# Performance work log

Measured on AMD Instinct MI355X. Metric: run time of the kernel, lower is better.

Reference implementation:

```python
import jax, jax.numpy as jnp
import numpy as np

NL = 4      # num_hidden_layers
NH = 12     # self-attn heads
CH = 4      # cross-attn heads (hardcoded in module)
S = 4       # speakers per dialog
EPS = 1e-5

def layernorm(x, g, b):
    m = x.mean(-1, keepdims=True)
    v = jnp.mean((x - m) ** 2, axis=-1, keepdims=True)
    return (x - m) * jax.lax.rsqrt(v + EPS) * g + b

def self_mha(x, in_w, in_b, out_w, out_b):
    # x: [B,T,L,H] self-attention over L (the per-turn token axis)
    B, T, L, H = x.shape
    dh = H // NH
    qkv = x @ in_w + in_b                       # [B,T,L,3H]
    q, k, v = jnp.split(qkv, 3, axis=-1)
    q = q.reshape(B, T, L, NH, dh); k = k.reshape(B, T, L, NH, dh); v = v.reshape(B, T, L, NH, dh)
    s = jnp.einsum('btqhd,btkhd->bthqk', q, k) / np.sqrt(dh).astype(x.dtype)
    a = jax.nn.softmax(s, axis=-1)
    o = jnp.einsum('bthqk,btkhd->btqhd', a, v).reshape(B, T, L, H)
    return o @ out_w + out_b

def forward(input_ids, attention_mask, speaker_ids, tok_emb, pos_emb, turn_emb,
            mha_in_w, mha_in_b, mha_out_w, mha_out_b,
            ffn_w1, ffn_b1, ffn_w2, ffn_b2,
            ln1_g, ln1_b, ln2_g, ln2_b,
            gate_w, gate_b, sn_g, sn_b,
            ca_in_w, ca_in_b, ca_out_w, ca_out_b):
    B, T, L = input_ids.shape
    H = tok_emb.shape[1]
    X = tok_emb[input_ids] + pos_emb[jnp.arange(L)][None, None] + turn_emb[jnp.arange(T)][None, :, None]
    mask = attention_mask[..., None].astype(X.dtype)            # [B,T,L,1]
    onehot = (speaker_ids[..., None] == jnp.arange(S)).astype(X.dtype)  # [B,T,S]
    counts = onehot.sum(1)                                      # [B,S]
    M = jnp.zeros((B, S, H), X.dtype)                           # speaker memory
    for l in range(NL):
        m_t = jnp.einsum('bts,bsh->bth', onehot, M)             # gather memory per turn
        h = (X + m_t[:, :, None, :]) * mask                     # mask applied by zeroing inputs (as in source)
        h = self_mha(h, mha_in_w[l], mha_in_b[l], mha_out_w[l], mha_out_b[l])
        h = layernorm(h + X, ln1_g[l], ln1_b[l])
        ffn = jax.nn.gelu(h @ ffn_w1[l] + ffn_b1[l], approximate=False) @ ffn_w2[l] + ffn_b2[l]
        h = layernorm(h + ffn, ln2_g[l], ln2_b[l])
        X = h
        tc = h.mean(2)                                          # token_context [B,T,H]
        # cross-attention: each turn's context queries its dialog's speaker memory
        wq, wk, wv = jnp.split(ca_in_w[l], 3, axis=-1)
        bq, bk, bv = jnp.split(ca_in_b[l], 3)
        dh = H // CH
        q = (tc @ wq + bq).reshape(B, T, CH, dh)
        k = (M @ wk + bk).reshape(B, S, CH, dh)
        v = (M @ wv + bv).reshape(B, S, CH, dh)
        s = jnp.einsum('bthd,bshd->bhts', q, k) / np.sqrt(dh).astype(X.dtype)
        a = jax.nn.softmax(s, axis=-1)
        cc = jnp.einsum('bhts,bshd->bthd', a, v).reshape(B, T, H) @ ca_out_w[l] + ca_out_b[l]
        fused = jnp.concatenate([tc, m_t, cc], axis=-1)         # [B,T,3H]
        upd = layernorm(fused @ gate_w[l] + gate_b[l] + m_t, sn_g[l], sn_b[l])
        # scatter: per-speaker mean over that speaker's turns; untouched speakers keep old memory
        sums = jnp.einsum('bts,bth->bsh', onehot, upd)
        mean = sums / jnp.maximum(counts, 1.0)[..., None]
        M = jnp.where((counts > 0)[..., None], mean, M)
    return X, M

def setup_inputs() -> dict:
    key = jax.random.key(0)
    ks = iter(jax.random.split(key, 32))
    B, T, L, H, F, V, P = 8, 64, 64, 768, 3072, 30522, 512
    n = lambda shape: jax.random.normal(next(ks), shape, jnp.float32) * 0.02
    return {
        'input_ids': jax.random.randint(next(ks), (B, T, L), 0, V, jnp.int32),
        'attention_mask': jax.random.randint(next(ks), (B, T, L), 0, 2, jnp.int32),
        'speaker_ids': jax.random.randint(next(ks), (B, T), 0, S, jnp.int32),
        'tok_emb': n((V, H)), 'pos_emb': n((P, H)), 'turn_emb': n((P, H)),
        'mha_in_w': n((NL, H, 3 * H)), 'mha_in_b': jnp.zeros((NL, 3 * H)),
        'mha_out_w': n((NL, H, H)), 'mha_out_b': jnp.zeros((NL, H)),
        'ffn_w1': n((NL, H, F)), 'ffn_b1': jnp.zeros((NL, F)),
        'ffn_w2': n((NL, F, H)), 'ffn_b2': jnp.zeros((NL, H)),
        'ln1_g': jnp.ones((NL, H)), 'ln1_b': jnp.zeros((NL, H)),
        'ln2_g': jnp.ones((NL, H)), 'ln2_b': jnp.zeros((NL, H)),
        'gate_w': n((NL, 3 * H, H)), 'gate_b': jnp.zeros((NL, H)),
        'sn_g': jnp.ones((NL, H)), 'sn_b': jnp.zeros((NL, H)),
        'ca_in_w': n((NL, H, 3 * H)), 'ca_in_b': jnp.zeros((NL, 3 * H)),
        'ca_out_w': n((NL, H, H)), 'ca_out_b': jnp.zeros((NL, H)),
    }

def reference(input_ids, attention_mask, speaker_ids, tok_emb, pos_emb, turn_emb,
              mha_in_w, mha_in_b, mha_out_w, mha_out_b,
              ffn_w1, ffn_b1, ffn_w2, ffn_b2,
              ln1_g, ln1_b, ln2_g, ln2_b,
              gate_w, gate_b, sn_g, sn_b,
              ca_in_w, ca_in_b, ca_out_w, ca_out_b):
    return forward(input_ids, attention_mask, speaker_ids, tok_emb, pos_emb, turn_emb,
                   mha_in_w, mha_in_b, mha_out_w, mha_out_b,
                   ffn_w1, ffn_b1, ffn_w2, ffn_b2,
                   ln1_g, ln1_b, ln2_g, ln2_b,
                   gate_w, gate_b, sn_g, sn_b,
                   ca_in_w, ca_in_b, ca_out_w, ca_out_b)
```

## Files before the change

kernel.cpp:

```cpp
#include <hip/hip_runtime.h>

using u16 = unsigned short;
using u32 = unsigned int;

#define DI __device__ __forceinline__

typedef __bf16 bf16x8 __attribute__((ext_vector_type(8)));
typedef float  f32x4  __attribute__((ext_vector_type(4)));

DI float b2f(u16 u){ u32 x = ((u32)u) << 16; float f; __builtin_memcpy(&f, &x, 4); return f; }
DI u16 f2b(float f){ __bf16 h = (__bf16)f; u16 r; __builtin_memcpy(&r, &h, 2); return r; }
DI float gelu_fast(float v){
    float u = v * (0.7978845608f + 0.0356774081f * v * v);
    float e = __expf(2.0f * u);
    float t = 1.0f - 2.0f / (e + 1.0f);
    return 0.5f * v * (1.0f + t);
}

#define GLOAD16(g, l) __builtin_amdgcn_global_load_lds( \
    (const __attribute__((address_space(1))) void*)(g), \
    (__attribute__((address_space(3))) void*)(l), 16, 0, 0)

DI bf16x8 ldsr128(const u16* p) {
    bf16x8 r;
    asm volatile("ds_read_b128 %0, %1"
                 : "=v"(r)
                 : "v"((const __attribute__((address_space(3))) u16*)p));
    return r;
}

template<int EPI>
__global__ __launch_bounds__(512, 1)
void gemm256(const u16* __restrict__ A, const u16* __restrict__ Bt,
             const float* __restrict__ bias, void* __restrict__ Cout,
             int M, int N, int K)
{
    __shared__ u16 lA[2][256 * 64];
    __shared__ u16 lB[2][256 * 64];
    const int tid  = threadIdx.x;
    const int lane = tid & 63;
    const int w    = tid >> 6;
    const int wm   = w >> 2, wn = w & 3;

    const int nx = gridDim.x;
    const int nb = nx * gridDim.y;
    int bid = blockIdx.y * nx + blockIdx.x;
    if ((nb & 7) == 0) bid = ((bid & 7) * (nb >> 3)) + (bid >> 3);
    const int m0 = (bid / nx) * 256;
    const int n0 = (bid % nx) * 256;

    f32x4 acc[8][4] = {};

    const int srowb = w * 32 + (lane >> 3);
    const int csrc  = ((lane & 7) ^ ((lane >> 3) & 7)) * 8;
    const u16* gA[4];
    const u16* gB[4];
    #pragma unroll
    for (int i = 0; i < 4; ++i) {
        int ra = m0 + srowb + i * 8; if (ra > M - 1) ra = M - 1;
        gA[i] = A  + (size_t)ra * K + csrc;
        gB[i] = Bt + (size_t)(n0 + srowb + i * 8) * K + csrc;
    }

    const int la = lane & 15, lg = lane >> 4;
    const int nt = K >> 6;

    #define STAGE(buf, k0) do { \
        _Pragma("unroll") \
        for (int i = 0; i < 4; ++i) { \
            GLOAD16(gA[i] + (k0), &lA[buf][(w * 256 + i * 64 + lane) * 8]); \
            GLOAD16(gB[i] + (k0), &lB[buf][(w * 256 + i * 64 + lane) * 8]); \
        } \
    } while (0)

    STAGE(0, 0);

    int cur = 0;
    for (int t = 0; t < nt; ++t) {
        asm volatile("s_waitcnt vmcnt(0)" ::: "memory");
        __builtin_amdgcn_s_barrier();
        asm volatile("" ::: "memory");

        if (t + 1 < nt) STAGE(cur ^ 1, (t + 1) << 6);

        #pragma unroll
        for (int ks = 0; ks < 2; ++ks) {
            bf16x8 af[8], bfr[4];
            #pragma unroll
            for (int i = 0; i < 8; i++)
                af[i] = ldsr128(&lA[cur][(wm * 128 + i * 16 + la) * 64
                                         + (((ks * 4 + lg) ^ (la & 7)) * 8)]);
            #pragma unroll
            for (int j = 0; j < 4; j++)
                bfr[j] = ldsr128(&lB[cur][(wn * 64 + j * 16 + la) * 64
                                          + (((ks * 4 + lg) ^ (la & 7)) * 8)]);
            asm volatile("s_waitcnt lgkmcnt(0)" ::: "memory");
            __builtin_amdgcn_sched_barrier(0);

            __builtin_amdgcn_s_setprio(1);
            #pragma unroll
            for (int i = 0; i < 8; i++)
                #pragma unroll
                for (int j = 0; j < 4; j++)
                    acc[i][j] = __builtin_amdgcn_mfma_f32_16x16x32_bf16(af[i], bfr[j], acc[i][j], 0, 0, 0);
            __builtin_amdgcn_s_setprio(0);
        }

        cur ^= 1;
    }
    #undef STAGE

    #pragma unroll
    for (int i = 0; i < 8; i++) {
        const int rowb = m0 + wm * 128 + i * 16 + lg * 4;
        #pragma unroll
        for (int j = 0; j < 4; j++) {
            const int col = n0 + wn * 64 + j * 16 + la;
            const float bv = bias[col];
            #pragma unroll
            for (int r = 0; r < 4; r++) {
                const int rr = rowb + r;
                if (rr < M) {
                    float v = acc[i][j][r] + bv;
                    if constexpr (EPI == 1) v = gelu_fast(v);
                    if constexpr (EPI == 2) ((float*)Cout)[(size_t)rr * N + col] = v;
                    else                    ((u16*)Cout)[(size_t)rr * N + col] = f2b(v);
                }
            }
        }
    }
}

template<int EPI>
__global__ __launch_bounds__(256)
void gemm_bt(const u16* __restrict__ A, const u16* __restrict__ Bt,
             const float* __restrict__ bias, void* __restrict__ Cout,
             int M, int N, int K)
{
    __shared__ u16 lA[3][128 * 32];
    __shared__ u16 lB[3][128 * 32];
    const int tid  = threadIdx.x;
    const int lane = tid & 63;
    const int w    = tid >> 6;
    const int wm   = w >> 1, wn = w & 1;

    const int nx = gridDim.x;
    const int nb = nx * gridDim.y;
    int bid = blockIdx.y * nx + blockIdx.x;
    if ((nb & 7) == 0) bid = ((bid & 7) * (nb >> 3)) + (bid >> 3);
    const int m0 = (bid / nx) * 128;
    const int n0 = (bid % nx) * 128;

    f32x4 acc[4][4] = {};

    const int srow = tid >> 2;
    const int scol = (((tid & 3) ^ ((tid >> 3) & 3)) * 8);
    int ar0 = m0 + srow;      if (ar0 > M - 1) ar0 = M - 1;
    int ar1 = m0 + 64 + srow; if (ar1 > M - 1) ar1 = M - 1;
    const u16* gA0 = A  + (size_t)ar0 * K + scol;
    const u16* gA1 = A  + (size_t)ar1 * K + scol;
    const u16* gB0 = Bt + (size_t)(n0 + srow) * K + scol;
    const u16* gB1 = Bt + (size_t)(n0 + 64 + srow) * K + scol;

    const int la = lane & 15, lg = lane >> 4;
    const int cp = (lg ^ ((la >> 1) & 3)) * 8;

    const int nt = K >> 5;

    GLOAD16(gA0,      &lA[0][tid * 8]);
    GLOAD16(gA1,      &lA[0][tid * 8 + 2048]);
    GLOAD16(gB0,      &lB[0][tid * 8]);
    GLOAD16(gB1,      &lB[0][tid * 8 + 2048]);
    GLOAD16(gA0 + 32, &lA[1][tid * 8]);
    GLOAD16(gA1 + 32, &lA[1][tid * 8 + 2048]);
    GLOAD16(gB0 + 32, &lB[1][tid * 8]);
    GLOAD16(gB1 + 32, &lB[1][tid * 8 + 2048]);

    int cur = 0, pre = 2;
    for (int t = 0; t < nt; ++t) {
        if (t + 1 < nt) asm volatile("s_waitcnt vmcnt(4)" ::: "memory");
        else            asm volatile("s_waitcnt vmcnt(0)" ::: "memory");
        __builtin_amdgcn_s_barrier();
        asm volatile("" ::: "memory");

        if (t + 2 < nt) {
            const int k0 = (t + 2) << 5;
            GLOAD16(gA0 + k0, &lA[pre][tid * 8]);
            GLOAD16(gA1 + k0, &lA[pre][tid * 8 + 2048]);
            GLOAD16(gB0 + k0, &lB[pre][tid * 8]);
            GLOAD16(gB1 + k0, &lB[pre][tid * 8 + 2048]);
        }

        bf16x8 af[4], bfr[4];
        #pragma unroll
        for (int i = 0; i < 4; i++)
            af[i] = ldsr128(&lA[cur][(wm * 64 + i * 16 + la) * 32 + cp]);
        #pragma unroll
        for (int j = 0; j < 4; j++)
            bfr[j] = ldsr128(&lB[cur][(wn * 64 + j * 16 + la) * 32 + cp]);
        asm volatile("s_waitcnt lgkmcnt(0)" ::: "memory");
        __builtin_amdgcn_sched_barrier(0);

        #pragma unroll
        for (int i = 0; i < 4; i++)
            #pragma unroll
            for (int j = 0; j < 4; j++)
                acc[i][j] = __builtin_amdgcn_mfma_f32_16x16x32_bf16(af[i], bfr[j], acc[i][j], 0, 0, 0);

        cur = (cur == 2) ? 0 : cur + 1;
        pre = (pre == 2) ? 0 : pre + 1;
    }

    #pragma unroll
    for (int i = 0; i < 4; i++) {
        const int rowb = m0 + wm * 64 + i * 16 + lg * 4;
        #pragma unroll
        for (int j = 0; j < 4; j++) {
            const int col = n0 + wn * 64 + j * 16 + la;
            const float bv = bias[col];
            #pragma unroll
            for (int r = 0; r < 4; r++) {
                const int rr = rowb + r;
                if (rr < M) {
                    float v = acc[i][j][r] + bv;
                    if constexpr (EPI == 1) v = gelu_fast(v);
                    if constexpr (EPI == 2) ((float*)Cout)[(size_t)rr * N + col] = v;
                    else                    ((u16*)Cout)[(size_t)rr * N + col] = f2b(v);
                }
            }
        }
    }
}

__global__ __launch_bounds__(256)
void transp_conv(const float* __restrict__ in, u16* __restrict__ out, int K, int N)
{
    __shared__ float tile[32][33];
    const int l = blockIdx.z;
    const float* inp = in + (size_t)l * K * N;
    u16* op = out + (size_t)l * K * N;
    const int kb = blockIdx.y * 32, nb = blockIdx.x * 32;
    const int tx = threadIdx.x, ty = threadIdx.y;
    #pragma unroll
    for (int i = 0; i < 32; i += 8)
        tile[ty + i][tx] = inp[(size_t)(kb + ty + i) * N + nb + tx];
    __syncthreads();
    #pragma unroll
    for (int i = 0; i < 32; i += 8)
        op[(size_t)(nb + ty + i) * K + kb + tx] = f2b(tile[tx][ty + i]);
}

__global__ __launch_bounds__(192)
void embed_k(const int* __restrict__ ids, const float* __restrict__ te,
             const float* __restrict__ pe, const float* __restrict__ ue,
             u16* __restrict__ X)
{
    const int tok = blockIdx.x;
    const int l = tok & 63;
    const int t = (tok >> 6) & 63;
    const int id = ids[tok];
    const int c = threadIdx.x * 4;
    float4 a = *(const float4*)&te[(size_t)id * 768 + c];
    float4 p = *(const float4*)&pe[(size_t)l * 768 + c];
    float4 u = *(const float4*)&ue[(size_t)t * 768 + c];
    ushort4 o;
    o.x = f2b(a.x + p.x + u.x); o.y = f2b(a.y + p.y + u.y);
    o.z = f2b(a.z + p.z + u.z); o.w = f2b(a.w + p.w + u.w);
    *(ushort4*)&X[(size_t)tok * 768 + c] = o;
}

__global__ __launch_bounds__(256)
void gather_mt(const float* __restrict__ M, const int* __restrict__ sid,
               float* __restrict__ mt)
{
    const int bt = blockIdx.x, b = bt >> 6, tid = threadIdx.x;
    const float* src = M + ((size_t)b * 4 + sid[bt]) * 768;
    float* dst = mt + (size_t)bt * 768;
    dst[tid] = src[tid]; dst[tid + 256] = src[tid + 256]; dst[tid + 512] = src[tid + 512];
}

__global__ __launch_bounds__(192)
void prep_ain(const u16* __restrict__ X, const float* __restrict__ mt,
              const int* __restrict__ mask, u16* __restrict__ Ain)
{
    const int tok = blockIdx.x, bt = tok >> 6;
    const float mk = (float)mask[tok];
    const int c = threadIdx.x * 4;
    ushort4 xv = *(const ushort4*)&X[(size_t)tok * 768 + c];
    float4 mv = *(const float4*)&mt[(size_t)bt * 768 + c];
    ushort4 o;
    o.x = f2b((b2f(xv.x) + mv.x) * mk); o.y = f2b((b2f(xv.y) + mv.y) * mk);
    o.z = f2b((b2f(xv.z) + mv.z) * mk); o.w = f2b((b2f(xv.w) + mv.w) * mk);
    *(ushort4*)&Ain[(size_t)tok * 768 + c] = o;
}

DI int swz(int row, int col) { return row * 64 + (((col >> 3) ^ (row & 7)) << 3) + (col & 7); }

__global__ __launch_bounds__(256)
void attn_self(const u16* __restrict__ QKV, u16* __restrict__ O)
{
    __shared__ u16 lQ[64 * 64], lK[64 * 64], lVt[64 * 64], lP[64 * 64];
    __shared__ float lS[64 * 68];
    const int bt = blockIdx.x / 12, h = blockIdx.x % 12;
    const int tid = threadIdx.x, lane = tid & 63, w = tid >> 6;
    const size_t base = (size_t)bt * 64 * 2304;

    #pragma unroll
    for (int it = 0; it < 2; ++it) {
        const int slot = it * 256 + tid;
        const int l = slot >> 3, dc = (slot & 7) * 8;
        const u16* qp = QKV + base + (size_t)l * 2304 + h * 64 + dc;
        *(uint4*)&lQ[swz(l, dc)] = *(const uint4*)qp;
        *(uint4*)&lK[swz(l, dc)] = *(const uint4*)(qp + 768);
        uint4 vv = *(const uint4*)(qp + 1536);
        u16 tmp[8]; *(uint4*)tmp = vv;
        #pragma unroll
        for (int j = 0; j < 8; j++) lVt[swz(dc + j, l)] = tmp[j];
    }
    __syncthreads();

    const int la = lane & 15, lg = lane >> 4;
    {
        f32x4 sa[4] = {};
        #pragma unroll
        for (int kh = 0; kh < 64; kh += 32) {
            bf16x8 aq = *(const bf16x8*)&lQ[swz(w * 16 + la, kh + lg * 8)];
            #pragma unroll
            for (int fn = 0; fn < 4; ++fn) {
                bf16x8 bk = *(const bf16x8*)&lK[swz(fn * 16 + la, kh + lg * 8)];
                sa[fn] = __builtin_amdgcn_mfma_f32_16x16x32_bf16(aq, bk, sa[fn], 0, 0, 0);
            }
        }
        #pragma unroll
        for (int fn = 0; fn < 4; ++fn)
            #pragma unroll
            for (int r = 0; r < 4; ++r)
                lS[(w * 16 + lg * 4 + r) * 68 + fn * 16 + la] = sa[fn][r] * 0.125f;
    }
    __syncthreads();

    {
        const int row = tid >> 2, q4 = tid & 3;
        float e[16]; float mx = -1e30f;
        #pragma unroll
        for (int j = 0; j < 16; j++) { e[j] = lS[row * 68 + q4 * 16 + j]; mx = fmaxf(mx, e[j]); }
        mx = fmaxf(mx, __shfl_xor(mx, 1)); mx = fmaxf(mx, __shfl_xor(mx, 2));
        float sm = 0.f;
        #pragma unroll
        for (int j = 0; j < 16; j++) { e[j] = __expf(e[j] - mx); sm += e[j]; }
        sm += __shfl_xor(sm, 1); sm += __shfl_xor(sm, 2);
        const float inv = 1.0f / sm;
        #pragma unroll
        for (int j = 0; j < 16; j++) lP[swz(row, q4 * 16 + j)] = f2b(e[j] * inv);
    }
    __syncthreads();

    {
        f32x4 oa[4] = {};
        #pragma unroll
        for (int kh = 0; kh < 64; kh += 32) {
            bf16x8 ap = *(const bf16x8*)&lP[swz(w * 16 + la, kh + lg * 8)];
            #pragma unroll
            for (int fn = 0; fn < 4; ++fn) {
                bf16x8 bv = *(const bf16x8*)&lVt[swz(fn * 16 + la, kh + lg * 8)];
                oa[fn] = __builtin_amdgcn_mfma_f32_16x16x32_bf16(ap, bv, oa[fn], 0, 0, 0);
            }
        }
        const size_t ob = (size_t)bt * 64 * 768 + h * 64;
        #pragma unroll
        for (int fn = 0; fn < 4; ++fn)
            #pragma unroll
            for (int r = 0; r < 4; ++r)
                O[ob + (size_t)(w * 16 + lg * 4 + r) * 768 + fn * 16 + la] = f2b(oa[fn][r]);
    }
}

DI float wave_red(float v) {
    #pragma unroll
    for (int o = 32; o > 0; o >>= 1) v += __shfl_xor(v, o);
    return v;
}

__global__ __launch_bounds__(256)
void ln_res(const u16* __restrict__ a, const u16* __restrict__ b,
            const float* __restrict__ g, const float* __restrict__ be,
            u16* __restrict__ out)
{
    __shared__ float red[8];
    const int tid = threadIdx.x;
    const size_t off = (size_t)blockIdx.x * 768;
    float x0 = b2f(a[off + tid])       + b2f(b[off + tid]);
    float x1 = b2f(a[off + tid + 256]) + b2f(b[off + tid + 256]);
    float x2 = b2f(a[off + tid + 512]) + b2f(b[off + tid + 512]);
    float s = wave_red(x0 + x1 + x2);
    float ss = wave_red(x0 * x0 + x1 * x1 + x2 * x2);
    if ((tid & 63) == 0) { red[tid >> 6] = s; red[4 + (tid >> 6)] = ss; }
    __syncthreads();
    s = red[0] + red[1] + red[2] + red[3];
    ss = red[4] + red[5] + red[6] + red[7];
    const float mean = s * (1.f / 768.f);
    const float var = fmaxf(ss * (1.f / 768.f) - mean * mean, 0.f);
    const float inv = rsqrtf(var + 1e-5f);
    out[off + tid]       = f2b((x0 - mean) * inv * g[tid]       + be[tid]);
    out[off + tid + 256] = f2b((x1 - mean) * inv * g[tid + 256] + be[tid + 256]);
    out[off + tid + 512] = f2b((x2 - mean) * inv * g[tid + 512] + be[tid + 512]);
}

__global__ __launch_bounds__(256)
void ln_upd(const float* __restrict__ a, const float* __restrict__ b,
            const float* __restrict__ g, const float* __restrict__ be,
            float* __restrict__ out)
{
    __shared__ float red[8];
    const int tid = threadIdx.x;
    const size_t off = (size_t)blockIdx.x * 768;
    float x0 = a[off + tid]       + b[off + tid];
    float x1 = a[off + tid + 256] + b[off + tid + 256];
    float x2 = a[off + tid + 512] + b[off + tid + 512];
    float s = wave_red(x0 + x1 + x2);
    float ss = wave_red(x0 * x0 + x1 * x1 + x2 * x2);
    if ((tid & 63) == 0) { red[tid >> 6] = s; red[4 + (tid >> 6)] = ss; }
    __syncthreads();
    s = red[0] + red[1] + red[2] + red[3];
    ss = red[4] + red[5] + red[6] + red[7];
    const float mean = s * (1.f / 768.f);
    const float var = fmaxf(ss * (1.f / 768.f) - mean * mean, 0.f);
    const float inv = rsqrtf(var + 1e-5f);
    out[off + tid]       = (x0 - mean) * inv * g[tid]       + be[tid];
    out[off + tid + 256] = (x1 - mean) * inv * g[tid + 256] + be[tid + 256];
    out[off + tid + 512] = (x2 - mean) * inv * g[tid + 512] + be[tid + 512];
}

__global__ __launch_bounds__(256)
void tc_mean(const u16* __restrict__ X, u16* __restrict__ tcb)
{
    const int bt = blockIdx.x, tid = threadIdx.x;
    float s0 = 0, s1 = 0, s2 = 0;
    for (int l = 0; l < 64; ++l) {
        const u16* r = X + ((size_t)bt * 64 + l) * 768;
        s0 += b2f(r[tid]); s1 += b2f(r[tid + 256]); s2 += b2f(r[tid + 512]);
    }
    tcb[(size_t)bt * 768 + tid]       = f2b(s0 * (1.f / 64.f));
    tcb[(size_t)bt * 768 + tid + 256] = f2b(s1 * (1.f / 64.f));
    tcb[(size_t)bt * 768 + tid + 512] = f2b(s2 * (1.f / 64.f));
}

__global__ __launch_bounds__(256)
void conv_bf16(const float* __restrict__ in, u16* __restrict__ out, int n)
{
    const int i = blockIdx.x * 256 + threadIdx.x;
    if (i < n) out[i] = f2b(in[i]);
}

__global__ __launch_bounds__(256)
void zero_f32(float* __restrict__ buf, int n)
{
    const int i = blockIdx.x * 256 + threadIdx.x;
    if (i < n) buf[i] = 0.f;
}

__global__ __launch_bounds__(256)
void cross_attn(const u16* __restrict__ qc, const u16* __restrict__ kvc,
                u16* __restrict__ cca)
{
    __shared__ float q[768], kk[4][768], vv[4][768], sraw[16], aw[16];
    const int bt = blockIdx.x, b = bt >> 6, tid = threadIdx.x;
    #pragma unroll
    for (int i = 0; i < 3; i++) q[tid + i * 256] = b2f(qc[(size_t)bt * 768 + tid + i * 256]);
    #pragma unroll
    for (int i = 0; i < 12; i++) {
        const int idx = i * 256 + tid;
        const int s = idx / 768, d = idx % 768;
        kk[s][d] = b2f(kvc[(size_t)(b * 4 + s) * 1536 + d]);
        vv[s][d] = b2f(kvc[(size_t)(b * 4 + s) * 1536 + 768 + d]);
    }
    __syncthreads();
    if (tid < 16) {
        const int hh = tid >> 2, s = tid & 3;
        float acc = 0.f;
        for (int d = 0; d < 192; ++d) acc += q[hh * 192 + d] * kk[s][hh * 192 + d];
        sraw[tid] = acc * 0.07216878364870323f;
    }
    __syncthreads();
    if (tid < 4) {
        float m = -1e30f;
        for (int s = 0; s < 4; s++) m = fmaxf(m, sraw[tid * 4 + s]);
        float ee[4], sm = 0.f;
        for (int s = 0; s < 4; s++) { ee[s] = __expf(sraw[tid * 4 + s] - m); sm += ee[s]; }
        for (int s = 0; s < 4; s++) aw[tid * 4 + s] = ee[s] / sm;
    }
    __syncthreads();
    #pragma unroll
    for (int i = 0; i < 3; i++) {
        const int j = tid + i * 256;
        const int hh = j / 192;
        float v = aw[hh * 4 + 0] * vv[0][j] + aw[hh * 4 + 1] * vv[1][j]
                + aw[hh * 4 + 2] * vv[2][j] + aw[hh * 4 + 3] * vv[3][j];
        cca[(size_t)bt * 768 + j] = f2b(v);
    }
}

__global__ __launch_bounds__(256)
void concat_fused(const u16* __restrict__ tcb, const float* __restrict__ mt,
                  const u16* __restrict__ ccp, u16* __restrict__ Fu)
{
    const int bt = blockIdx.x, tid = threadIdx.x;
    u16* o = Fu + (size_t)bt * 2304;
    #pragma unroll
    for (int i = 0; i < 3; i++) {
        const int j = tid + i * 256;
        o[j]        = tcb[(size_t)bt * 768 + j];
        o[768 + j]  = f2b(mt[(size_t)bt * 768 + j]);
        o[1536 + j] = ccp[(size_t)bt * 768 + j];
    }
}

__global__ __launch_bounds__(256)
void scatter_mem(const float* __restrict__ upd, const int* __restrict__ sid,
                 const float* __restrict__ counts, float* __restrict__ M)
{
    const int bs = blockIdx.x, b = bs >> 2, s = bs & 3, tid = threadIdx.x;
    const float c = counts[bs];
    #pragma unroll
    for (int i = 0; i < 3; i++) {
        const int j = tid + i * 256;
        float acc = 0.f;
        for (int t = 0; t < 64; ++t)
            if (sid[b * 64 + t] == s) acc += upd[((size_t)b * 64 + t) * 768 + j];
        if (c > 0.f) M[(size_t)bs * 768 + j] = acc / fmaxf(c, 1.f);
    }
}

__global__ void calc_counts(const int* __restrict__ sid, float* __restrict__ counts)
{
    const int tid = threadIdx.x;
    if (tid < 32) {
        const int b = tid >> 2, s = tid & 3;
        float c = 0.f;
        for (int t = 0; t < 64; ++t) c += (sid[b * 64 + t] == s) ? 1.f : 0.f;
        counts[tid] = c;
    }
}

__global__ __launch_bounds__(256)
void final_out(const u16* __restrict__ Xb, const float* __restrict__ M,
               float* __restrict__ out)
{
    const size_t i = (size_t)blockIdx.x * 256 + threadIdx.x;
    const size_t NX = 25165824ull;
    if (i < NX) out[i] = b2f(Xb[i]);
    else if (i < NX + 24576ull) out[i] = M[i - NX];
}

extern "C" void kernel_launch(void* const* d_in, const int* in_sizes, int n_in,
                              void* d_out, int out_size, void* d_ws, size_t ws_size,
                              hipStream_t stream)
{
    const int*   input_ids = (const int*)d_in[0];
    const int*   attn_mask = (const int*)d_in[1];
    const int*   sid       = (const int*)d_in[2];
    const float* tok_emb   = (const float*)d_in[3];
    const float* pos_emb   = (const float*)d_in[4];
    const float* turn_emb  = (const float*)d_in[5];
    const float* mha_in_w  = (const float*)d_in[6];
    const float* mha_in_b  = (const float*)d_in[7];
    const float* mha_out_w = (const float*)d_in[8];
    const float* mha_out_b = (const float*)d_in[9];
    const float* ffn_w1    = (const float*)d_in[10];
    const float* ffn_b1    = (const float*)d_in[11];
    const float* ffn_w2    = (const float*)d_in[12];
    const float* ffn_b2    = (const float*)d_in[13];
    const float* ln1_g     = (const float*)d_in[14];
    const float* ln1_b     = (const float*)d_in[15];
    const float* ln2_g     = (const float*)d_in[16];
    const float* ln2_b     = (const float*)d_in[17];
    const float* gate_w    = (const float*)d_in[18];
    const float* gate_b    = (const float*)d_in[19];
    const float* sn_g      = (const float*)d_in[20];
    const float* sn_b      = (const float*)d_in[21];
    const float* ca_in_w   = (const float*)d_in[22];
    const float* ca_in_b   = (const float*)d_in[23];
    const float* ca_out_w  = (const float*)d_in[24];
    const float* ca_out_b  = (const float*)d_in[25];
    (void)in_sizes; (void)n_in; (void)out_size;

    const size_t MB = 1ull << 20;
    int NCA, NCF; bool allW;
    if      (ws_size >= 460 * MB) { NCA = 2; NCF = 1; allW = true;  }
    else if (ws_size >= 255 * MB) { NCA = 2; NCF = 2; allW = false; }
    else                          { NCA = 4; NCF = 4; allW = false; }
    const int MRA = 32768 / NCA;
    const int MRF = 32768 / NCF;
    const size_t wl = allW ? 4 : 1;

    char* p = (char*)d_ws;
    auto alloc = [&](size_t n) { void* r = p; p += (n + 255) & ~(size_t)255; return r; };
    u16*   Xb    = (u16*)alloc(50331648);
    u16*   Hb    = (u16*)alloc(50331648);
    u16*   WqkvT = (u16*)alloc(wl * 3538944);
    u16*   WoT   = (u16*)alloc(wl * 1179648);
    u16*   W1T   = (u16*)alloc(wl * 4718592);
    u16*   W2T   = (u16*)alloc(wl * 4718592);
    u16*   WgT   = (u16*)alloc(wl * 3538944);
    u16*   WcaT  = (u16*)alloc(wl * 3538944);
    u16*   WcoT  = (u16*)alloc(wl * 1179648);
    float* mt    = (float*)alloc(1572864);
    u16*   tcb   = (u16*)alloc(786432);
    u16*   Mb    = (u16*)alloc(49152);
    u16*   qc    = (u16*)alloc(786432);
    u16*   kvc   = (u16*)alloc(98304);
    u16*   cca   = (u16*)alloc(786432);
    u16*   ccp   = (u16*)alloc(786432);
    u16*   Fu    = (u16*)alloc(2359296);
    float* gout  = (float*)alloc(1572864);
    float* upd   = (float*)alloc(1572864);
    float* cnts  = (float*)alloc(256);
    float* M     = (float*)alloc(98304);

    u16 *A, *QKVb, *Gb;
    if (NCF == 1) {
        A    = (u16*)alloc(50331648);
        Gb   = (u16*)alloc(201326592);
        QKVb = (u16*)d_out;
    } else if (NCF == 2) {
        A    = (u16*)alloc(50331648);
        QKVb = (u16*)alloc((size_t)MRA * 2304 * 2);
        Gb   = (u16*)d_out;
    } else {
        Gb   = (u16*)alloc((size_t)MRF * 3072 * 2);
        A    = (u16*)d_out;
        QKVb = (u16*)d_out + 25165824;
    }
    u16* Obuf = Gb;

    zero_f32<<<96, 256, 0, stream>>>(M, 24576);
    calc_counts<<<1, 64, 0, stream>>>(sid, cnts);
    embed_k<<<32768, 192, 0, stream>>>(input_ids, tok_emb, pos_emb, turn_emb, Xb);

    if (allW) {
        transp_conv<<<dim3(72, 24, 4), dim3(32, 8), 0, stream>>>(mha_in_w,  WqkvT, 768, 2304);
        transp_conv<<<dim3(24, 24, 4), dim3(32, 8), 0, stream>>>(mha_out_w, WoT,   768, 768);
        transp_conv<<<dim3(96, 24, 4), dim3(32, 8), 0, stream>>>(ffn_w1,    W1T,   768, 3072);
        transp_conv<<<dim3(24, 96, 4), dim3(32, 8), 0, stream>>>(ffn_w2,    W2T,  3072, 768);
        transp_conv<<<dim3(24, 72, 4), dim3(32, 8), 0, stream>>>(gate_w,    WgT,  2304, 768);
        transp_conv<<<dim3(72, 24, 4), dim3(32, 8), 0, stream>>>(ca_in_w,   WcaT,  768, 2304);
        transp_conv<<<dim3(24, 24, 4), dim3(32, 8), 0, stream>>>(ca_out_w,  WcoT,  768, 768);
    }

    for (int l = 0; l < 4; ++l) {
        if (!allW) {
            transp_conv<<<dim3(72, 24), dim3(32, 8), 0, stream>>>(mha_in_w  + (size_t)l * 768 * 2304, WqkvT, 768, 2304);
            transp_conv<<<dim3(24, 24), dim3(32, 8), 0, stream>>>(mha_out_w + (size_t)l * 768 * 768,  WoT,   768, 768);
            transp_conv<<<dim3(96, 24), dim3(32, 8), 0, stream>>>(ffn_w1    + (size_t)l * 768 * 3072, W1T,   768, 3072);
            transp_conv<<<dim3(24, 96), dim3(32, 8), 0, stream>>>(ffn_w2    + (size_t)l * 3072 * 768, W2T,  3072, 768);
            transp_conv<<<dim3(24, 72), dim3(32, 8), 0, stream>>>(gate_w    + (size_t)l * 2304 * 768, WgT,  2304, 768);
            transp_conv<<<dim3(72, 24), dim3(32, 8), 0, stream>>>(ca_in_w   + (size_t)l * 768 * 2304, WcaT,  768, 2304);
            transp_conv<<<dim3(24, 24), dim3(32, 8), 0, stream>>>(ca_out_w  + (size_t)l * 768 * 768,  WcoT,  768, 768);
        }
        const u16* Wqkv_l = WqkvT + (size_t)(allW ? l : 0) * 2304 * 768;
        const u16* Wo_l   = WoT   + (size_t)(allW ? l : 0) * 768 * 768;
        const u16* W1_l   = W1T   + (size_t)(allW ? l : 0) * 768 * 3072;
        const u16* W2_l   = W2T   + (size_t)(allW ? l : 0) * 3072 * 768;
        const u16* Wg_l   = WgT   + (size_t)(allW ? l : 0) * 2304 * 768;
        const u16* Wca_l  = WcaT  + (size_t)(allW ? l : 0) * 768 * 2304;
        const u16* Wco_l  = WcoT  + (size_t)(allW ? l : 0) * 768 * 768;

        gather_mt<<<512, 256, 0, stream>>>(M, sid, mt);
        prep_ain<<<32768, 192, 0, stream>>>(Xb, mt, attn_mask, A);

        for (int c = 0; c < NCA; ++c) {
            u16* Ac = A + (size_t)c * MRA * 768;
            gemm256<0><<<dim3(9, MRA / 256), 512, 0, stream>>>(Ac, Wqkv_l, mha_in_b + l * 2304, QKVb, MRA, 2304, 768);
            attn_self<<<(MRA / 64) * 12, 256, 0, stream>>>(QKVb, Obuf);
            gemm256<0><<<dim3(3, MRA / 256), 512, 0, stream>>>(Obuf, Wo_l, mha_out_b + l * 768, Ac, MRA, 768, 768);
        }
        ln_res<<<32768, 256, 0, stream>>>(A, Xb, ln1_g + l * 768, ln1_b + l * 768, Hb);

        for (int c = 0; c < NCF; ++c) {
            u16* Hc = Hb + (size_t)c * MRF * 768;
            u16* Ac = A  + (size_t)c * MRF * 768;
            gemm256<1><<<dim3(12, MRF / 256), 512, 0, stream>>>(Hc, W1_l, ffn_b1 + l * 3072, Gb, MRF, 3072, 768);
            gemm256<0><<<dim3(3, MRF / 256), 512, 0, stream>>>(Gb, W2_l, ffn_b2 + l * 768, Ac, MRF, 768, 3072);
        }
        ln_res<<<32768, 256, 0, stream>>>(A, Hb, ln2_g + l * 768, ln2_b + l * 768, Xb);

        tc_mean<<<512, 256, 0, stream>>>(Xb, tcb);
        conv_bf16<<<96, 256, 0, stream>>>(M, Mb, 24576);
        gemm_bt<0><<<dim3(6, 4), 256, 0, stream>>>(tcb, Wca_l, ca_in_b + l * 2304, qc, 512, 768, 768);
        gemm_bt<0><<<dim3(12, 1), 256, 0, stream>>>(Mb, Wca_l + 768 * 768, ca_in_b + l * 2304 + 768, kvc, 32, 1536, 768);
        cross_attn<<<512, 256, 0, stream>>>(qc, kvc, cca);
        gemm_bt<0><<<dim3(6, 4), 256, 0, stream>>>(cca, Wco_l, ca_out_b + l * 768, ccp, 512, 768, 768);
        concat_fused<<<512, 256, 0, stream>>>(tcb, mt, ccp, Fu);
        gemm_bt<2><<<dim3(6, 4), 256, 0, stream>>>(Fu, Wg_l, gate_b + l * 768, gout, 512, 768, 2304);
        ln_upd<<<512, 256, 0, stream>>>(gout, mt, sn_g + l * 768, sn_b + l * 768, upd);
        scatter_mem<<<32, 256, 0, stream>>>(upd, sid, cnts, M);
    }

    final_out<<<98400, 256, 0, stream>>>(Xb, M, (float*)d_out);
}
```

Before: 4.208 ms.

## Interleave LDS reads, global prefetch and MFMA in phased GEMM loop; use smaller tiles for N=768

Restructures the 256x256 GEMM main loop into four phases per K-tile. Each phase loads a slice of A fragments from LDS and issues part of the next tile's global-to-LDS prefetch, then runs its MFMAs, with barriers between phases to keep waves in lockstep. The aim is to overlap LDS reads and global loads with matrix math and cut fragment register pressure. Separately, the N=768 output-projection and FFN-down GEMMs now use the 128-tile gemm_bt kernel, which launches more blocks for those narrow shapes. The extra barriers per phase add synchronization overhead.

```diff
diff --git a/kernel.cpp b/kernel.cpp
--- a/kernel.cpp
+++ b/kernel.cpp
@@ -31,9 +31,9 @@
 
 template<int EPI>
 __global__ __launch_bounds__(512, 1)
-void gemm256(const u16* __restrict__ A, const u16* __restrict__ Bt,
-             const float* __restrict__ bias, void* __restrict__ Cout,
-             int M, int N, int K)
+void gemm256p(const u16* __restrict__ A, const u16* __restrict__ Bt,
+              const float* __restrict__ bias, void* __restrict__ Cout,
+              int M, int N, int K)
 {
     __shared__ u16 lA[2][256 * 64];
     __shared__ u16 lB[2][256 * 64];
@@ -65,50 +65,72 @@
     const int la = lane & 15, lg = lane >> 4;
     const int nt = K >> 6;
 
-    #define STAGE(buf, k0) do { \
-        _Pragma("unroll") \
-        for (int i = 0; i < 4; ++i) { \
-            GLOAD16(gA[i] + (k0), &lA[buf][(w * 256 + i * 64 + lane) * 8]); \
-            GLOAD16(gB[i] + (k0), &lB[buf][(w * 256 + i * 64 + lane) * 8]); \
-        } \
-    } while (0)
-
-    STAGE(0, 0);
-
-    int cur = 0;
+    #pragma unroll
+    for (int i = 0; i < 4; ++i) GLOAD16(gA[i], &lA[0][(w * 256 + i * 64 + lane) * 8]);
+    #pragma unroll
+    for (int i = 0; i < 4; ++i) GLOAD16(gB[i], &lB[0][(w * 256 + i * 64 + lane) * 8]);
+    asm volatile("s_waitcnt vmcnt(0)" ::: "memory");
+    __builtin_amdgcn_s_barrier();
+    asm volatile("" ::: "memory");
+
     for (int t = 0; t < nt; ++t) {
-        asm volatile("s_waitcnt vmcnt(0)" ::: "memory");
-        __builtin_amdgcn_s_barrier();
-        asm volatile("" ::: "memory");
-
-        if (t + 1 < nt) STAGE(cur ^ 1, (t + 1) << 6);
-
-        #pragma unroll
-        for (int ks = 0; ks < 2; ++ks) {
-            bf16x8 af[8], bfr[4];
-            #pragma unroll
-            for (int i = 0; i < 8; i++)
-                af[i] = ldsr128(&lA[cur][(wm * 128 + i * 16 + la) * 64
-                                         + (((ks * 4 + lg) ^ (la & 7)) * 8)]);
-            #pragma unroll
-            for (int j = 0; j < 4; j++)
-                bfr[j] = ldsr128(&lB[cur][(wn * 64 + j * 16 + la) * 64
-                                          + (((ks * 4 + lg) ^ (la & 7)) * 8)]);
+        const int p = t & 1;
+        const u16* lAp = lA[p];
+        const u16* lBp = lB[p];
+        u16* dA = lA[p ^ 1];
+        u16* dB = lB[p ^ 1];
+        const int kn = (t + 1) << 6;
+        const bool more = (t + 1 < nt);
+
+        bf16x8 bf[4][2];
+
+        #pragma unroll
+        for (int ph = 0; ph < 4; ++ph) {
+            if (ph == 0) {
+                #pragma unroll
+                for (int j = 0; j < 4; ++j) {
+                    bf[j][0] = ldsr128(&lBp[(wn * 64 + j * 16 + la) * 64 + (((0 * 4 + lg) ^ (la & 7)) * 8)]);
+                    bf[j][1] = ldsr128(&lBp[(wn * 64 + j * 16 + la) * 64 + (((1 * 4 + lg) ^ (la & 7)) * 8)]);
+                }
+            }
+            bf16x8 a0k0 = ldsr128(&lAp[(wm * 128 + (2 * ph) * 16 + la) * 64     + (((0 * 4 + lg) ^ (la & 7)) * 8)]);
+            bf16x8 a0k1 = ldsr128(&lAp[(wm * 128 + (2 * ph) * 16 + la) * 64     + (((1 * 4 + lg) ^ (la & 7)) * 8)]);
+            bf16x8 a1k0 = ldsr128(&lAp[(wm * 128 + (2 * ph + 1) * 16 + la) * 64 + (((0 * 4 + lg) ^ (la & 7)) * 8)]);
+            bf16x8 a1k1 = ldsr128(&lAp[(wm * 128 + (2 * ph + 1) * 16 + la) * 64 + (((1 * 4 + lg) ^ (la & 7)) * 8)]);
+
+            if (ph == 0 && more) {
+                #pragma unroll
+                for (int i = 0; i < 4; ++i) GLOAD16(gA[i] + kn, &dA[(w * 256 + i * 64 + lane) * 8]);
+            }
+            if (ph == 1 && more) {
+                #pragma unroll
+                for (int i = 0; i < 4; ++i) GLOAD16(gB[i] + kn, &dB[(w * 256 + i * 64 + lane) * 8]);
+            }
+
+            __builtin_amdgcn_s_barrier();
             asm volatile("s_waitcnt lgkmcnt(0)" ::: "memory");
             __builtin_amdgcn_sched_barrier(0);
 
             __builtin_amdgcn_s_setprio(1);
             #pragma unroll
-            for (int i = 0; i < 8; i++)
-                #pragma unroll
-                for (int j = 0; j < 4; j++)
-                    acc[i][j] = __builtin_amdgcn_mfma_f32_16x16x32_bf16(af[i], bfr[j], acc[i][j], 0, 0, 0);
+            for (int j = 0; j < 4; ++j) {
+                acc[2 * ph][j]     = __builtin_amdgcn_mfma_f32_16x16x32_bf16(a0k0, bf[j][0], acc[2 * ph][j],     0, 0, 0);
+                acc[2 * ph + 1][j] = __builtin_amdgcn_mfma_f32_16x16x32_bf16(a1k0, bf[j][0], acc[2 * ph + 1][j], 0, 0, 0);
+            }
+            #pragma unroll
+            for (int j = 0; j < 4; ++j) {
+                acc[2 * ph][j]     = __builtin_amdgcn_mfma_f32_16x16x32_bf16(a0k1, bf[j][1], acc[2 * ph][j],     0, 0, 0);
+                acc[2 * ph + 1][j] = __builtin_amdgcn_mfma_f32_16x16x32_bf16(a1k1, bf[j][1], acc[2 * ph + 1][j], 0, 0, 0);
+            }
             __builtin_amdgcn_s_setprio(0);
-        }
-
-        cur ^= 1;
-    }
-    #undef STAGE
+
+            if (ph == 3) {
+                asm volatile("s_waitcnt vmcnt(0)" ::: "memory");
+            }
+            __builtin_amdgcn_s_barrier();
+            asm volatile("" ::: "memory");
+        }
+    }
 
     #pragma unroll
     for (int i = 0; i < 8; i++) {
@@ -670,17 +692,17 @@
 
         for (int c = 0; c < NCA; ++c) {
             u16* Ac = A + (size_t)c * MRA * 768;
-            gemm256<0><<<dim3(9, MRA / 256), 512, 0, stream>>>(Ac, Wqkv_l, mha_in_b + l * 2304, QKVb, MRA, 2304, 768);
+            gemm256p<0><<<dim3(9, MRA / 256), 512, 0, stream>>>(Ac, Wqkv_l, mha_in_b + l * 2304, QKVb, MRA, 2304, 768);
             attn_self<<<(MRA / 64) * 12, 256, 0, stream>>>(QKVb, Obuf);
-            gemm256<0><<<dim3(3, MRA / 256), 512, 0, stream>>>(Obuf, Wo_l, mha_out_b + l * 768, Ac, MRA, 768, 768);
+            gemm_bt<0><<<dim3(6, MRA / 128), 256, 0, stream>>>(Obuf, Wo_l, mha_out_b + l * 768, Ac, MRA, 768, 768);
         }
         ln_res<<<32768, 256, 0, stream>>>(A, Xb, ln1_g + l * 768, ln1_b + l * 768, Hb);
 
         for (int c = 0; c < NCF; ++c) {
             u16* Hc = Hb + (size_t)c * MRF * 768;
             u16* Ac = A  + (size_t)c * MRF * 768;
-            gemm256<1><<<dim3(12, MRF / 256), 512, 0, stream>>>(Hc, W1_l, ffn_b1 + l * 3072, Gb, MRF, 3072, 768);
-            gemm256<0><<<dim3(3, MRF / 256), 512, 0, stream>>>(Gb, W2_l, ffn_b2 + l * 768, Ac, MRF, 768, 3072);
+            gemm256p<1><<<dim3(12, MRF / 256), 512, 0, stream>>>(Hc, W1_l, ffn_b1 + l * 3072, Gb, MRF, 3072, 768);
+            gemm_bt<0><<<dim3(6, MRF / 128), 256, 0, stream>>>(Gb, W2_l, ffn_b2 + l * 768, Ac, MRF, 768, 3072);
         }
         ln_res<<<32768, 256, 0, stream>>>(A, Hb, ln2_g + l * 768, ln2_b + l * 768, Xb);
 
```

Result: no change. 4.228 ms (+0.5%).
